# Kernel tuning notes

Hardware: AMD Instinct MI355X
Metric: run time of the kernel (lower is better)

Reference implementation:

```python
import jax, jax.numpy as jnp
import numpy as np

SCALE = 11.313708498984761  # sqrt(d_k=128)


def setup_inputs() -> dict:
    key = jax.random.key(0)
    kq, kk, kv = jax.random.split(key, 3)
    B, N, D = 32, 2048, 128
    q = jax.random.normal(kq, (B, N, D), dtype=jnp.float32)
    k = jax.random.normal(kk, (B, N, D), dtype=jnp.float32)
    v = jax.random.normal(kv, (B, N, D), dtype=jnp.float32)
    # causal mask: True = masked (matches torch masked_fill semantics)
    causal = jnp.triu(jnp.ones((N, N), dtype=jnp.bool_), k=1)
    mask = jnp.broadcast_to(causal, (B, N, N))
    return {"q": q, "k": k, "v": v, "mask": mask}


def reference(q, k, v, mask):
    # scores: [B, N, N]
    u = jnp.einsum("bnd,bmd->bnm", q, k) / SCALE
    u = jnp.where(mask, -jnp.inf, u)
    attn = jax.nn.softmax(u, axis=2)
    output = jnp.einsum("bnm,bmd->bnd", attn, v)
    return (attn, output)
```

## Files before the change

kernel.cpp:

```cpp
#include <hip/hip_runtime.h>

#define Nn 2048
#define Dd 128
#define BM 64
#define BN 64
#define QS 68
#define VS 36

typedef __attribute__((ext_vector_type(8))) short short8;
typedef __attribute__((ext_vector_type(4))) float f32x4;
typedef __attribute__((ext_vector_type(2))) unsigned int u32x2;
typedef __attribute__((ext_vector_type(4))) unsigned int u32x4;

__device__ __forceinline__ unsigned int pack2(float x, float y){
  unsigned int ux = __float_as_uint(x);
  ux += 0x7fffu + ((ux >> 16) & 1u);
  unsigned int uy = __float_as_uint(y);
  uy += 0x7fffu + ((uy >> 16) & 1u);
  return (ux >> 16) | (uy & 0xffff0000u);
}

extern "C" __global__ void __launch_bounds__(256, 3)
attn_kernel(const float* __restrict__ qg, const float* __restrict__ kg,
            const float* __restrict__ vg, float* __restrict__ attn,
            float* __restrict__ outp)
{
  __shared__ unsigned int Qs[BM * QS];
  __shared__ unsigned int Ks[BN * QS];
  __shared__ unsigned int Vt[Dd * VS];

  const int tid  = threadIdx.x;
  const int x    = (int)gridDim.x - 1 - (int)blockIdx.x;
  const int b    = blockIdx.y;
  const int n0   = x * BM;
  const int T    = x + 1;
  const int lane = tid & 63;
  const int wv   = tid >> 6;
  const int a    = lane & 15;
  const int q    = lane >> 4;
  const int rloc = wv * 16 + a;
  const float inv_scale = 0.08838834764831845f;

  {
    const int row = tid >> 2, qt = tid & 3;
    const float* src = qg + ((size_t)b * Nn + n0 + row) * Dd + qt * 32;
    unsigned int* dst = &Qs[row * QS + qt * 16];
    #pragma unroll
    for (int j = 0; j < 4; ++j){
      const f32x4 a0 = *(const f32x4*)(src + j * 8);
      const f32x4 a1 = *(const f32x4*)(src + j * 8 + 4);
      u32x4 wd;
      wd.x = pack2(a0.x, a0.y); wd.y = pack2(a0.z, a0.w);
      wd.z = pack2(a1.x, a1.y); wd.w = pack2(a1.z, a1.w);
      *(u32x4*)(dst + j * 4) = wd;
    }
  }

  const int krow = tid >> 2, kqt = tid & 3;
  f32x4 kb[8];
  auto loadK = [&](int tk){
    const float* s = kg + ((size_t)b * Nn + (size_t)tk * BN + krow) * Dd + kqt * 32;
    #pragma unroll
    for (int j = 0; j < 8; ++j) kb[j] = *(const f32x4*)(s + j * 4);
  };
  auto storeK = [&](){
    unsigned int* dst = &Ks[krow * QS + kqt * 16];
    #pragma unroll
    for (int j = 0; j < 4; ++j){
      u32x4 wd;
      wd.x = pack2(kb[2*j].x,   kb[2*j].y);
      wd.y = pack2(kb[2*j].z,   kb[2*j].w);
      wd.z = pack2(kb[2*j+1].x, kb[2*j+1].y);
      wd.w = pack2(kb[2*j+1].z, kb[2*j+1].w);
      *(u32x4*)(dst + j * 4) = wd;
    }
  };

  float lp = 0.0f;
  loadK(0);
  for (int tk = 0; tk < T; ++tk){
    __syncthreads();
    storeK();
    __syncthreads();
    if (tk + 1 < T) loadK(tk + 1);

    f32x4 acc[4];
    #pragma unroll
    for (int tc = 0; tc < 4; ++tc) acc[tc] = (f32x4)0.0f;
    #pragma unroll
    for (int kk = 0; kk < 4; ++kk){
      const short8 qf = __builtin_bit_cast(short8,
          *(const u32x4*)&Qs[rloc * QS + kk * 16 + q * 4]);
      #pragma unroll
      for (int tc = 0; tc < 4; ++tc){
        const short8 kf = __builtin_bit_cast(short8,
            *(const u32x4*)&Ks[(tc * 16 + a) * QS + kk * 16 + q * 4]);
        acc[tc] = __builtin_amdgcn_mfma_f32_16x16x32_bf16(kf, qf, acc[tc], 0, 0, 0);
      }
    }
    if (tk == x){
      #pragma unroll
      for (int tc = 0; tc < 4; ++tc)
        #pragma unroll
        for (int r = 0; r < 4; ++r){
          const int col = tc * 16 + q * 4 + r;
          if (col <= rloc) lp += __expf(acc[tc][r] * inv_scale);
        }
    } else {
      #pragma unroll
      for (int tc = 0; tc < 4; ++tc)
        #pragma unroll
        for (int r = 0; r < 4; ++r)
          lp += __expf(acc[tc][r] * inv_scale);
    }
  }
  lp += __shfl_xor(lp, 16);
  lp += __shfl_xor(lp, 32);
  const float rl = 1.0f / lp;

  f32x4 acco[8];
  #pragma unroll
  for (int tc = 0; tc < 8; ++tc) acco[tc] = (f32x4)0.0f;

  f32x4 vb[8];
  const int vmp = tid & 31, vd0 = (tid >> 5) * 16;
  auto loadV = [&](int tk){
    const float* s0 = vg + ((size_t)b * Nn + (size_t)tk * BN + 2 * vmp) * Dd + vd0;
    #pragma unroll
    for (int j = 0; j < 4; ++j){
      vb[j]     = *(const f32x4*)(s0 + j * 4);
      vb[4 + j] = *(const f32x4*)(s0 + Dd + j * 4);
    }
  };
  auto storeV = [&](){
    #pragma unroll
    for (int j = 0; j < 4; ++j){
      Vt[(vd0 + j*4 + 0) * VS + vmp] = pack2(vb[j].x, vb[4+j].x);
      Vt[(vd0 + j*4 + 1) * VS + vmp] = pack2(vb[j].y, vb[4+j].y);
      Vt[(vd0 + j*4 + 2) * VS + vmp] = pack2(vb[j].z, vb[4+j].z);
      Vt[(vd0 + j*4 + 3) * VS + vmp] = pack2(vb[j].w, vb[4+j].w);
    }
  };

  loadK(T - 1); loadV(T - 1);
  for (int i = 0; i < T; ++i){
    const int tk = T - 1 - i;
    __syncthreads();
    storeK(); storeV();
    __syncthreads();
    if (i + 1 < T){ loadK(tk - 1); loadV(tk - 1); }

    f32x4 acc[4];
    #pragma unroll
    for (int tc = 0; tc < 4; ++tc) acc[tc] = (f32x4)0.0f;
    #pragma unroll
    for (int kk = 0; kk < 4; ++kk){
      const short8 qf = __builtin_bit_cast(short8,
          *(const u32x4*)&Qs[rloc * QS + kk * 16 + q * 4]);
      #pragma unroll
      for (int tc = 0; tc < 4; ++tc){
        const short8 kf = __builtin_bit_cast(short8,
            *(const u32x4*)&Ks[(tc * 16 + a) * QS + kk * 16 + q * 4]);
        acc[tc] = __builtin_amdgcn_mfma_f32_16x16x32_bf16(kf, qf, acc[tc], 0, 0, 0);
      }
    }

    const bool diag = (tk == x);
    const size_t arow = ((size_t)b * Nn + n0 + rloc) * (size_t)Nn + (size_t)tk * BN;
    unsigned int Wp[4][2];
    #pragma unroll
    for (int tc = 0; tc < 4; ++tc){
      f32x4 p;
      #pragma unroll
      for (int r = 0; r < 4; ++r){
        const int col = tc * 16 + q * 4 + r;
        float e = __expf(acc[tc][r] * inv_scale) * rl;
        if (diag && col > rloc) e = 0.0f;
        p[r] = e;
      }
      *(f32x4*)(attn + arow + tc * 16 + q * 4) = p;
      Wp[tc][0] = pack2(p.x, p.y);
      Wp[tc][1] = pack2(p.z, p.w);
    }

    #pragma unroll
    for (int kk = 0; kk < 2; ++kk){
      u32x4 F;
      #pragma unroll
      for (int j = 0; j < 4; ++j){
        const int src = (((2 * q + (j >> 1)) & 3) << 4) | a;
        const unsigned int v0 = (unsigned int)__shfl((int)Wp[kk*2 + 0][j & 1], src, 64);
        const unsigned int v1 = (unsigned int)__shfl((int)Wp[kk*2 + 1][j & 1], src, 64);
        F[j] = (q & 2) ? v1 : v0;
      }
      const short8 pf = __builtin_bit_cast(short8, F);
      #pragma unroll
      for (int tc = 0; tc < 8; ++tc){
        const short8 vf = __builtin_bit_cast(short8,
            *(const u32x4*)&Vt[(tc * 16 + a) * VS + kk * 16 + q * 4]);
        acco[tc] = __builtin_amdgcn_mfma_f32_16x16x32_bf16(pf, vf, acco[tc], 0, 0, 0);
      }
    }
  }

  {
    float* orow = outp + ((size_t)b * Nn + n0) * Dd;
    #pragma unroll
    for (int tc = 0; tc < 8; ++tc)
      #pragma unroll
      for (int r = 0; r < 4; ++r)
        orow[(size_t)(wv * 16 + q * 4 + r) * Dd + tc * 16 + a] = acco[tc][r];
  }

  {
    const int mEnd = T * BN;
    float* zrow = attn + ((size_t)b * Nn + n0 + (tid >> 2)) * (size_t)Nn;
    const f32x4 z = (f32x4)0.0f;
    for (int cc = mEnd + (tid & 3) * 4; cc < Nn; cc += 16)
      *(f32x4*)(zrow + cc) = z;
  }
}

extern "C" void kernel_launch(void* const* d_in, const int* in_sizes, int n_in,
                              void* d_out, int out_size, void* d_ws, size_t ws_size,
                              hipStream_t stream) {
  const float* q = (const float*)d_in[0];
  const float* k = (const float*)d_in[1];
  const float* v = (const float*)d_in[2];
  float* attn = (float*)d_out;
  float* out  = attn + (size_t)32 * Nn * Nn;
  dim3 grid(32, 32), block(256);
  attn_kernel<<<grid, block, 0, stream>>>(q, k, v, attn, out);
  (void)in_sizes; (void)n_in; (void)out_size; (void)d_ws; (void)ws_size;
}
```

Baseline: 1.209 ms.

## Load Q/K fragments directly from global into registers; double-buffer V in LDS

Removes the Q and K shared-memory staging. Q fragments are held in registers for the whole kernel, and K fragments are read from global memory (relying on L1/L2 across the four waves) and packed to bf16 right before each MFMA. V is double-buffered in LDS so each tile needs one barrier instead of two. The smaller LDS footprint allows launch bounds of 4 blocks per CU. The cost is redundant global K loads per wave and exposed load latency in front of the MFMAs, since K is no longer prefetched.

```diff
diff --git a/kernel.cpp b/kernel.cpp
--- a/kernel.cpp
+++ b/kernel.cpp
@@ -4,7 +4,6 @@
 #define Dd 128
 #define BM 64
 #define BN 64
-#define QS 68
 #define VS 36
 
 typedef __attribute__((ext_vector_type(8))) short short8;
@@ -20,14 +19,12 @@
   return (ux >> 16) | (uy & 0xffff0000u);
 }
 
-extern "C" __global__ void __launch_bounds__(256, 3)
+extern "C" __global__ void __launch_bounds__(256, 4)
 attn_kernel(const float* __restrict__ qg, const float* __restrict__ kg,
             const float* __restrict__ vg, float* __restrict__ attn,
             float* __restrict__ outp)
 {
-  __shared__ unsigned int Qs[BM * QS];
-  __shared__ unsigned int Ks[BN * QS];
-  __shared__ unsigned int Vt[Dd * VS];
+  __shared__ unsigned int Vt[2][Dd * VS];
 
   const int tid  = threadIdx.x;
   const int x    = (int)gridDim.x - 1 - (int)blockIdx.x;
@@ -41,79 +38,63 @@
   const int rloc = wv * 16 + a;
   const float inv_scale = 0.08838834764831845f;
 
+  short8 qf[4];
   {
-    const int row = tid >> 2, qt = tid & 3;
-    const float* src = qg + ((size_t)b * Nn + n0 + row) * Dd + qt * 32;
-    unsigned int* dst = &Qs[row * QS + qt * 16];
-    #pragma unroll
-    for (int j = 0; j < 4; ++j){
-      const f32x4 a0 = *(const f32x4*)(src + j * 8);
-      const f32x4 a1 = *(const f32x4*)(src + j * 8 + 4);
-      u32x4 wd;
-      wd.x = pack2(a0.x, a0.y); wd.y = pack2(a0.z, a0.w);
-      wd.z = pack2(a1.x, a1.y); wd.w = pack2(a1.z, a1.w);
-      *(u32x4*)(dst + j * 4) = wd;
-    }
-  }
-
-  const int krow = tid >> 2, kqt = tid & 3;
-  f32x4 kb[8];
-  auto loadK = [&](int tk){
-    const float* s = kg + ((size_t)b * Nn + (size_t)tk * BN + krow) * Dd + kqt * 32;
-    #pragma unroll
-    for (int j = 0; j < 8; ++j) kb[j] = *(const f32x4*)(s + j * 4);
+    const float* qsrc = qg + ((size_t)b * Nn + n0 + rloc) * Dd;
+    #pragma unroll
+    for (int kk = 0; kk < 4; ++kk){
+      const f32x4 a0 = *(const f32x4*)(qsrc + kk * 32 + q * 8);
+      const f32x4 a1 = *(const f32x4*)(qsrc + kk * 32 + q * 8 + 4);
+      u32x4 w;
+      w.x = pack2(a0.x, a0.y); w.y = pack2(a0.z, a0.w);
+      w.z = pack2(a1.x, a1.y); w.w = pack2(a1.z, a1.w);
+      qf[kk] = __builtin_bit_cast(short8, w);
+    }
+  }
+
+  const float* kb0 = kg + (size_t)b * Nn * Dd;
+
+  auto qk_tile = [&](int tk, f32x4* acc){
+    const float* kt = kb0 + (size_t)tk * BN * Dd;
+    #pragma unroll
+    for (int kk = 0; kk < 4; ++kk){
+      #pragma unroll
+      for (int tc = 0; tc < 4; ++tc){
+        const float* s = kt + (tc * 16 + a) * Dd + kk * 32 + q * 8;
+        const f32x4 r0 = *(const f32x4*)s;
+        const f32x4 r1 = *(const f32x4*)(s + 4);
+        u32x4 w;
+        w.x = pack2(r0.x, r0.y); w.y = pack2(r0.z, r0.w);
+        w.z = pack2(r1.x, r1.y); w.w = pack2(r1.z, r1.w);
+        acc[tc] = __builtin_amdgcn_mfma_f32_16x16x32_bf16(
+            __builtin_bit_cast(short8, w), qf[kk], acc[tc], 0, 0, 0);
+      }
+    }
   };
-  auto storeK = [&](){
-    unsigned int* dst = &Ks[krow * QS + kqt * 16];
-    #pragma unroll
-    for (int j = 0; j < 4; ++j){
-      u32x4 wd;
-      wd.x = pack2(kb[2*j].x,   kb[2*j].y);
-      wd.y = pack2(kb[2*j].z,   kb[2*j].w);
-      wd.z = pack2(kb[2*j+1].x, kb[2*j+1].y);
-      wd.w = pack2(kb[2*j+1].z, kb[2*j+1].w);
-      *(u32x4*)(dst + j * 4) = wd;
-    }
-  };
-
-  float lp = 0.0f;
-  loadK(0);
+
+  f32x4 lpv = (f32x4)0.0f;
   for (int tk = 0; tk < T; ++tk){
-    __syncthreads();
-    storeK();
-    __syncthreads();
-    if (tk + 1 < T) loadK(tk + 1);
-
     f32x4 acc[4];
     #pragma unroll
     for (int tc = 0; tc < 4; ++tc) acc[tc] = (f32x4)0.0f;
-    #pragma unroll
-    for (int kk = 0; kk < 4; ++kk){
-      const short8 qf = __builtin_bit_cast(short8,
-          *(const u32x4*)&Qs[rloc * QS + kk * 16 + q * 4]);
-      #pragma unroll
-      for (int tc = 0; tc < 4; ++tc){
-        const short8 kf = __builtin_bit_cast(short8,
-            *(const u32x4*)&Ks[(tc * 16 + a) * QS + kk * 16 + q * 4]);
-        acc[tc] = __builtin_amdgcn_mfma_f32_16x16x32_bf16(kf, qf, acc[tc], 0, 0, 0);
-      }
-    }
+    qk_tile(tk, acc);
     if (tk == x){
       #pragma unroll
       for (int tc = 0; tc < 4; ++tc)
         #pragma unroll
         for (int r = 0; r < 4; ++r){
           const int col = tc * 16 + q * 4 + r;
-          if (col <= rloc) lp += __expf(acc[tc][r] * inv_scale);
+          if (col <= rloc) lpv[r] += __expf(acc[tc][r] * inv_scale);
         }
     } else {
       #pragma unroll
       for (int tc = 0; tc < 4; ++tc)
         #pragma unroll
         for (int r = 0; r < 4; ++r)
-          lp += __expf(acc[tc][r] * inv_scale);
-    }
-  }
+          lpv[r] += __expf(acc[tc][r] * inv_scale);
+    }
+  }
+  float lp = (lpv.x + lpv.y) + (lpv.z + lpv.w);
   lp += __shfl_xor(lp, 16);
   lp += __shfl_xor(lp, 32);
   const float rl = 1.0f / lp;
@@ -132,38 +113,31 @@
       vb[4 + j] = *(const f32x4*)(s0 + Dd + j * 4);
     }
   };
-  auto storeV = [&](){
+  auto storeV = [&](int bi){
+    unsigned int* B = &Vt[bi][0];
     #pragma unroll
     for (int j = 0; j < 4; ++j){
-      Vt[(vd0 + j*4 + 0) * VS + vmp] = pack2(vb[j].x, vb[4+j].x);
-      Vt[(vd0 + j*4 + 1) * VS + vmp] = pack2(vb[j].y, vb[4+j].y);
-      Vt[(vd0 + j*4 + 2) * VS + vmp] = pack2(vb[j].z, vb[4+j].z);
-      Vt[(vd0 + j*4 + 3) * VS + vmp] = pack2(vb[j].w, vb[4+j].w);
+      B[(vd0 + j*4 + 0) * VS + vmp] = pack2(vb[j].x, vb[4+j].x);
+      B[(vd0 + j*4 + 1) * VS + vmp] = pack2(vb[j].y, vb[4+j].y);
+      B[(vd0 + j*4 + 2) * VS + vmp] = pack2(vb[j].z, vb[4+j].z);
+      B[(vd0 + j*4 + 3) * VS + vmp] = pack2(vb[j].w, vb[4+j].w);
     }
   };
 
-  loadK(T - 1); loadV(T - 1);
+  int cur = 0;
+  loadV(T - 1);
+  storeV(0);
+  __syncthreads();
+
   for (int i = 0; i < T; ++i){
     const int tk = T - 1 - i;
-    __syncthreads();
-    storeK(); storeV();
-    __syncthreads();
-    if (i + 1 < T){ loadK(tk - 1); loadV(tk - 1); }
 
     f32x4 acc[4];
     #pragma unroll
     for (int tc = 0; tc < 4; ++tc) acc[tc] = (f32x4)0.0f;
-    #pragma unroll
-    for (int kk = 0; kk < 4; ++kk){
-      const short8 qf = __builtin_bit_cast(short8,
-          *(const u32x4*)&Qs[rloc * QS + kk * 16 + q * 4]);
-      #pragma unroll
-      for (int tc = 0; tc < 4; ++tc){
-        const short8 kf = __builtin_bit_cast(short8,
-            *(const u32x4*)&Ks[(tc * 16 + a) * QS + kk * 16 + q * 4]);
-        acc[tc] = __builtin_amdgcn_mfma_f32_16x16x32_bf16(kf, qf, acc[tc], 0, 0, 0);
-      }
-    }
+    qk_tile(tk, acc);
+
+    if (i + 1 < T) loadV(tk - 1);
 
     const bool diag = (tk == x);
     const size_t arow = ((size_t)b * Nn + n0 + rloc) * (size_t)Nn + (size_t)tk * BN;
@@ -197,9 +171,15 @@
       #pragma unroll
       for (int tc = 0; tc < 8; ++tc){
         const short8 vf = __builtin_bit_cast(short8,
-            *(const u32x4*)&Vt[(tc * 16 + a) * VS + kk * 16 + q * 4]);
+            *(const u32x4*)&Vt[cur][(tc * 16 + a) * VS + kk * 16 + q * 4]);
         acco[tc] = __builtin_amdgcn_mfma_f32_16x16x32_bf16(pf, vf, acco[tc], 0, 0, 0);
       }
+    }
+
+    if (i + 1 < T){
+      storeV(cur ^ 1);
+      __syncthreads();
+      cur ^= 1;
     }
   }
 
```

Result: slower. 1.747 ms (+44.5%).
